# Optimization experiments

Hardware: AMD Instinct MI355X
Metric: run time of the kernel (lower is better)

## Reference

```python
import jax, jax.numpy as jnp
import numpy as np

C = 256
C4 = C // 4  # 64
B = 4
N = 4096
FACTOR = float(np.sqrt(C4))


def setup_inputs() -> dict:
    key = jax.random.key(0)
    k1, k2, k3, k4 = jax.random.split(key, 4)
    x = jax.random.normal(k1, (B, C, N), dtype=jnp.float32)
    # q_conv and k_conv share the SAME weight (tied in the torch module)
    W_qk = jax.random.normal(k2, (C4, C), dtype=jnp.float32) * (1.0 / np.sqrt(C))
    W_v = jax.random.normal(k3, (C4, C), dtype=jnp.float32) * (1.0 / np.sqrt(C))
    b_v = jax.random.normal(k4, (C4,), dtype=jnp.float32) * 0.01
    return {"x": x, "W_qk": W_qk, "W_v": W_v, "b_v": b_v}


def reference(x, W_qk, W_v, b_v):
    # Conv1d with kernel size 1 == per-position linear: [B,C,N] -> [B,C4,N]
    x_q = jnp.einsum('oc,bcn->bon', W_qk, x)          # [B, C4, N]
    x_k = x_q                                          # tied weights: k == q
    x_v = jnp.einsum('oc,bcn->bon', W_v, x) + b_v[None, :, None]  # [B, C4, N]
    # energy = x_k.permute(0,2,1) @ x_q : [B, N, N]
    energy = jnp.einsum('bcn,bcm->bnm', x_k, x_q) / FACTOR
    attention = jax.nn.softmax(energy, axis=-1)        # softmax over last dim
    x_r = jnp.einsum('bcn,bnm->bcm', x_v, attention)   # [B, C4, N]
    return x_r
```

## Files before the change

### kernel.cpp

```cpp
#include <hip/hip_runtime.h>


#define CC 256
#define C4C 64
#define NBATCH 4
#define NN 4096
#define QSCALE 0.42466089f
#define SHIFT2 12.0f

typedef _Float16 f16;
typedef _Float16 half2v __attribute__((ext_vector_type(2)));
typedef _Float16 half4 __attribute__((ext_vector_type(4)));
typedef _Float16 half8 __attribute__((ext_vector_type(8)));
typedef __fp16 fp16x2 __attribute__((ext_vector_type(2)));
typedef float floatx4 __attribute__((ext_vector_type(4)));

static __device__ __forceinline__ half2v pkrtz(float a, float b) {
  fp16x2 r = __builtin_amdgcn_cvt_pkrtz(a, b);
  return __builtin_bit_cast(half2v, r);
}

#define LOADQ(T, A0, A1)                                                   \
  { const f16* p_ = Qb + (size_t)(T) * 1024 + l * 8;                       \
    A0 = *(const half8*)(p_); A1 = *(const half8*)(p_ + 512); }

#define XT_PITCH 264
__global__ __launch_bounds__(256) void qv_kernel(
    const float* __restrict__ x, const float* __restrict__ Wqk,
    const float* __restrict__ Wv, const float* __restrict__ bv,
    f16* __restrict__ Qtb, float* __restrict__ V)
{
  __shared__ __align__(16) f16 xt[32][XT_PITCH];
  const int b = blockIdx.y;
  const int n0 = blockIdx.x * 32;
  const int tid = threadIdx.x;

  {
    const int nq = tid & 7;
    const int cb = tid >> 3;
    const int c = cb * 8;
    const float* xp = x + (size_t)b * CC * NN + n0 + nq * 4;
    float4 r[8];
#pragma unroll
    for (int j = 0; j < 8; ++j)
      r[j] = *(const float4*)(xp + (size_t)(c + j) * NN);
#pragma unroll
    for (int s = 0; s < 4; ++s) {
      half8 h;
#pragma unroll
      for (int j = 0; j < 8; ++j) h[j] = (f16)(((const float*)&r[j])[s]);
      *(half8*)(&xt[nq * 4 + s][c]) = h;
    }
  }

  const int w = tid >> 6, l = tid & 63, lr = l & 15, lg = l >> 4;
  const float* Wsrc = (w < 2) ? Wqk : Wv;
  const int ocb = (w & 1) * 32;
  half8 af[2][8];
#pragma unroll
  for (int t = 0; t < 2; ++t) {
    const float* wp = Wsrc + (size_t)(ocb + t * 16 + lr) * CC + 8 * lg;
#pragma unroll
    for (int kk = 0; kk < 8; ++kk) {
      float4 wa = *(const float4*)(wp + kk * 32);
      float4 wb = *(const float4*)(wp + kk * 32 + 4);
      half8 h;
      h[0] = (f16)wa.x; h[1] = (f16)wa.y; h[2] = (f16)wa.z; h[3] = (f16)wa.w;
      h[4] = (f16)wb.x; h[5] = (f16)wb.y; h[6] = (f16)wb.z; h[7] = (f16)wb.w;
      af[t][kk] = h;
    }
  }

  __syncthreads();

  floatx4 acc[2][2] = {{{0.f,0.f,0.f,0.f},{0.f,0.f,0.f,0.f}},
                       {{0.f,0.f,0.f,0.f},{0.f,0.f,0.f,0.f}}};
#pragma unroll
  for (int nt = 0; nt < 2; ++nt) {
#pragma unroll
    for (int kk = 0; kk < 8; ++kk) {
      half8 bf = *(const half8*)(&xt[nt * 16 + lr][kk * 32 + 8 * lg]);
      acc[0][nt] = __builtin_amdgcn_mfma_f32_16x16x32_f16(af[0][kk], bf, acc[0][nt], 0, 0, 0);
      acc[1][nt] = __builtin_amdgcn_mfma_f32_16x16x32_f16(af[1][kk], bf, acc[1][nt], 0, 0, 0);
    }
  }

  if (w < 2) {
#pragma unroll
    for (int t = 0; t < 2; ++t)
#pragma unroll
      for (int nt = 0; nt < 2; ++nt) {
        int T = (n0 >> 4) + nt;
        int kg = 2 * t + (lg >> 1);
        union { f16 h[4]; unsigned long long u; } q4;
#pragma unroll
        for (int i = 0; i < 4; ++i) q4.h[i] = (f16)(acc[t][nt][i] * QSCALE);
        *(unsigned long long*)(Qtb + (size_t)(b * 256 + T) * 1024 + w * 512
                               + (kg * 16 + lr) * 8 + (lg & 1) * 4) = q4.u;
      }
  } else {
#pragma unroll
    for (int t = 0; t < 2; ++t)
#pragma unroll
      for (int nt = 0; nt < 2; ++nt) {
        int n = n0 + nt * 16 + lr;
        int oc = (w - 2) * 32 + t * 16 + 4 * lg;
#pragma unroll
        for (int i = 0; i < 4; ++i)
          V[((size_t)(b * C4C) + oc + i) * NN + n] = acc[t][nt][i] + bv[oc + i];
      }
  }
}

#define Z_PRELOAD(TBEG)                                                    \
  { _Pragma("unroll")                                                      \
    for (int mt = 0; mt < 8; ++mt) {                                       \
      const f16* p_ = Qb + (size_t)((TBEG) + mt) * 1024 + l * 8;           \
      bb[mt][0] = *(const half8*)(p_);                                     \
      bb[mt][1] = *(const half8*)(p_ + 512);                               \
    } }

#define Z_E(MT, D0, D1)                                                    \
  { D0 = (floatx4){0.f,0.f,0.f,0.f}; D1 = (floatx4){0.f,0.f,0.f,0.f};      \
    D0 = __builtin_amdgcn_mfma_f32_16x16x32_f16(a[0][0], bb[MT][0], D0, 0, 0, 0); \
    D1 = __builtin_amdgcn_mfma_f32_16x16x32_f16(a[1][0], bb[MT][0], D1, 0, 0, 0); \
    D0 = __builtin_amdgcn_mfma_f32_16x16x32_f16(a[0][1], bb[MT][1], D0, 0, 0, 0); \
    D1 = __builtin_amdgcn_mfma_f32_16x16x32_f16(a[1][1], bb[MT][1], D1, 0, 0, 0); }

#define Z_SM(D0, D1)                                                       \
  { _Pragma("unroll")                                                      \
    for (int i = 0; i < 4; ++i) {                                          \
      rs[0][i] += __builtin_amdgcn_exp2f(D0[i]);                           \
      rs[1][i] += __builtin_amdgcn_exp2f(D1[i]); } }

#define Z_TILES17                                                          \
  Z_E(1, dB0, dB1); Z_SM(dA0, dA1);                                        \
  Z_E(2, dA0, dA1); Z_SM(dB0, dB1);                                        \
  Z_E(3, dB0, dB1); Z_SM(dA0, dA1);                                        \
  Z_E(4, dA0, dA1); Z_SM(dB0, dB1);                                        \
  Z_E(5, dB0, dB1); Z_SM(dA0, dA1);                                        \
  Z_E(6, dA0, dA1); Z_SM(dB0, dB1);                                        \
  Z_E(7, dB0, dB1); Z_SM(dA0, dA1);

__global__ __launch_bounds__(256) void z_kernel(
    const f16* __restrict__ Qtb, float* __restrict__ Zp)
{
  __shared__ float zl[4][32];
  const int bx = blockIdx.x;
  const int xcd = bx & 7, slot = bx >> 3;
  const int b = xcd >> 1;
  const int wu = ((xcd & 1) << 7) | slot;
  const int n0 = (wu >> 1) * 32;
  const int mh = wu & 1;
  const int tid = threadIdx.x;
  const int w = tid >> 6, l = tid & 63, lr = l & 15, lg = l >> 4;
  const f16* Qb = Qtb + (size_t)b * 256 * 1024;

  half8 a[2][2];
  LOADQ((n0 >> 4), a[0][0], a[0][1]);
  LOADQ((n0 >> 4) + 1, a[1][0], a[1][1]);

  const int tstr = mh * 128 + w * 32;
  half8 bb[8][2];
  floatx4 dA0, dA1, dB0, dB1;
  float rs[2][4] = {{0.f,0.f,0.f,0.f},{0.f,0.f,0.f,0.f}};

  Z_PRELOAD(tstr);
  Z_E(0, dA0, dA1);
  Z_TILES17;
#pragma unroll 1
  for (int mch = 1; mch < 4; ++mch) {
    Z_PRELOAD(tstr + mch * 8);
    Z_SM(dB0, dB1);
    Z_E(0, dA0, dA1);
    Z_TILES17;
  }
  Z_SM(dB0, dB1);

#pragma unroll
  for (int t = 0; t < 2; ++t)
#pragma unroll
    for (int i = 0; i < 4; ++i) {
      float v = rs[t][i];
      v += __shfl_xor(v, 1); v += __shfl_xor(v, 2);
      v += __shfl_xor(v, 4); v += __shfl_xor(v, 8);
      rs[t][i] = v;
    }
  if (lr == 0) {
#pragma unroll
    for (int t = 0; t < 2; ++t)
#pragma unroll
      for (int i = 0; i < 4; ++i)
        zl[w][16 * t + 4 * lg + i] = rs[t][i];
  }
  __syncthreads();
  if (tid < 32) {
    float s = zl[0][tid] + zl[1][tid] + zl[2][tid] + zl[3][tid];
    Zp[(size_t)mh * NBATCH * NN + b * NN + n0 + tid] = s;
  }
}

__global__ __launch_bounds__(256) void zr_kernel(
    const float* __restrict__ Zp, float* __restrict__ Z)
{
  int i = blockIdx.x * 256 + threadIdx.x;
  Z[i] = Zp[i] + Zp[(size_t)NBATCH * NN + i];
}

__global__ __launch_bounds__(256) void u_kernel(
    const float* __restrict__ V, const float* __restrict__ Z,
    f16* __restrict__ U4)
{
  size_t t = (size_t)blockIdx.x * 256 + threadIdx.x;
  size_t e = t * 8;
  int b = (int)(e >> 18);
  int c = (int)((e >> 12) & 63);
  int n = (int)(e & (NN - 1));
  const float* vp = V + (size_t)b * C4C * NN + (size_t)c * NN + n;
  float4 v0 = *(const float4*)(vp);
  float4 v1 = *(const float4*)(vp + 4);
  const float* zp = Z + b * NN + n;
  float4 z0 = *(const float4*)(zp);
  float4 z1 = *(const float4*)(zp + 4);
  half2v h0 = pkrtz(v0.x * 4096.0f / z0.x, v0.y * 4096.0f / z0.y);
  half2v h1 = pkrtz(v0.z * 4096.0f / z0.z, v0.w * 4096.0f / z0.w);
  half2v h2 = pkrtz(v1.x * 4096.0f / z1.x, v1.y * 4096.0f / z1.y);
  half2v h3 = pkrtz(v1.z * 4096.0f / z1.z, v1.w * 4096.0f / z1.w);
  half8 h = {h0[0], h0[1], h1[0], h1[1], h2[0], h2[1], h3[0], h3[1]};
  *(half8*)(U4 + (size_t)b * (C4C * NN) + (size_t)(n >> 4) * 1024 + c * 16 + (n & 15)) = h;
}

#define LOADU(NB, UA)                                                      \
  { const f16* up_ = Ub + (size_t)(NB) * 1024 + 4 * lg;                    \
    _Pragma("unroll")                                                      \
    for (int cs = 0; cs < 4; ++cs)                                         \
      UA[cs] = *(const half4*)(up_ + (16 * cs + lr) * 16); }

__global__ __launch_bounds__(512, 4) void av_kernel(
    const f16* __restrict__ Qtb, const f16* __restrict__ U4,
    float* __restrict__ Out)
{
  __shared__ float red[8][2][16][17];

  const int bx = blockIdx.x;
  const int xcd = bx & 7, slot = bx >> 3;
  const int b = xcd >> 1;
  const int m0 = (((xcd & 1) << 6) | slot) * 32;
  const int tid = threadIdx.x;
  const int w = tid >> 6;
  const int l = tid & 63;
  const int lr = l & 15, lg = l >> 4;

  const f16* Qb = Qtb + (size_t)b * 256 * 1024;
  const f16* Ub = U4 + (size_t)b * (C4C * NN);

  half8 bq[2][2];
  LOADQ((m0 >> 4), bq[0][0], bq[0][1]);
  LOADQ((m0 >> 4) + 1, bq[1][0], bq[1][1]);

  floatx4 o[4][2];
#pragma unroll
  for (int cs = 0; cs < 4; ++cs)
#pragma unroll
    for (int t = 0; t < 2; ++t) o[cs][t] = (floatx4){0.f, 0.f, 0.f, 0.f};

#pragma unroll 2
  for (int it = 0; it < 32; ++it) {
    const int T = it * 8 + w;
    half8 a0, a1;
    LOADQ(T, a0, a1);
    half4 ua[4];
    LOADU(T, ua);

    floatx4 dA = {-SHIFT2, -SHIFT2, -SHIFT2, -SHIFT2};
    floatx4 dB = {-SHIFT2, -SHIFT2, -SHIFT2, -SHIFT2};
    dA = __builtin_amdgcn_mfma_f32_16x16x32_f16(a0, bq[0][0], dA, 0, 0, 0);
    dB = __builtin_amdgcn_mfma_f32_16x16x32_f16(a0, bq[1][0], dB, 0, 0, 0);
    dA = __builtin_amdgcn_mfma_f32_16x16x32_f16(a1, bq[0][1], dA, 0, 0, 0);
    dB = __builtin_amdgcn_mfma_f32_16x16x32_f16(a1, bq[1][1], dB, 0, 0, 0);

    half2v p0a = pkrtz(__builtin_amdgcn_exp2f(dA[0]), __builtin_amdgcn_exp2f(dA[1]));
    half2v p0b = pkrtz(__builtin_amdgcn_exp2f(dA[2]), __builtin_amdgcn_exp2f(dA[3]));
    half2v p1a = pkrtz(__builtin_amdgcn_exp2f(dB[0]), __builtin_amdgcn_exp2f(dB[1]));
    half2v p1b = pkrtz(__builtin_amdgcn_exp2f(dB[2]), __builtin_amdgcn_exp2f(dB[3]));
    half4 bt0 = {p0a[0], p0a[1], p0b[0], p0b[1]};
    half4 bt1 = {p1a[0], p1a[1], p1b[0], p1b[1]};
#pragma unroll
    for (int cs = 0; cs < 4; ++cs) {
      o[cs][0] = __builtin_amdgcn_mfma_f32_16x16x16f16(ua[cs], bt0, o[cs][0], 0, 0, 0);
      o[cs][1] = __builtin_amdgcn_mfma_f32_16x16x16f16(ua[cs], bt1, o[cs][1], 0, 0, 0);
    }
  }

#pragma unroll 1
  for (int cs = 0; cs < 4; ++cs) {
    __syncthreads();
#pragma unroll
    for (int t = 0; t < 2; ++t)
#pragma unroll
      for (int i = 0; i < 4; ++i)
        red[w][t][4 * lg + i][lr] = o[cs][t][i];
    __syncthreads();
    const int t = tid >> 8;
    const int r = (tid >> 4) & 15;
    const int col = tid & 15;
    float ssum = 0.f;
#pragma unroll
    for (int ww = 0; ww < 8; ++ww) ssum += red[ww][t][r][col];
    Out[((size_t)b * C4C + cs * 16 + r) * NN + m0 + t * 16 + col] = ssum;
  }
}

extern "C" void kernel_launch(void* const* d_in, const int* in_sizes, int n_in,
                              void* d_out, int out_size, void* d_ws, size_t ws_size,
                              hipStream_t stream)
{
  const float* x   = (const float*)d_in[0];
  const float* Wqk = (const float*)d_in[1];
  const float* Wv  = (const float*)d_in[2];
  const float* bv  = (const float*)d_in[3];
  float* out = (float*)d_out;

  char* ws = (char*)d_ws;
  f16*   Qtb = (f16*)(ws);
  float* V   = (float*)(ws + (2u << 20));
  float* Z   = (float*)(ws + (6u << 20));
  f16*   U4  = (f16*)(ws + (6u << 20) + (64u << 10));
  float* Zp  = (float*)(ws + (6u << 20) + (64u << 10));

  qv_kernel<<<dim3(128, 4), 256, 0, stream>>>(x, Wqk, Wv, bv, Qtb, V);
  z_kernel<<<dim3(1024), 256, 0, stream>>>(Qtb, Zp);
  zr_kernel<<<dim3(64), 256, 0, stream>>>(Zp, Z);
  u_kernel<<<dim3(512), 256, 0, stream>>>(V, Z, U4);
  av_kernel<<<dim3(512), 512, 0, stream>>>(Qtb, U4, out);
}
```

Before: 64.98 us.

## Retile z_kernel to 64 rows per block with four-way column split

Each z_kernel block now covers 64 query rows (four 16-row tiles held in registers) and a quarter of the key columns, instead of 32 rows and half the columns. Each loaded key tile is reused across four A tiles, which raises MFMA work per global load. The zr_kernel now sums four partial Z arrays instead of two. The explicit software pipelining of the MFMA and exp2 steps is dropped in favour of a simple loop, and more registers are held live, which could reduce overlap or occupancy.

After: 67.52 us. +3.9%, slower.

```diff
diff --git a/kernel.cpp b/kernel.cpp
--- a/kernel.cpp
+++ b/kernel.cpp
@@ -112,73 +112,55 @@
   }
 }
 
-#define Z_PRELOAD(TBEG)                                                    \
-  { _Pragma("unroll")                                                      \
-    for (int mt = 0; mt < 8; ++mt) {                                       \
-      const f16* p_ = Qb + (size_t)((TBEG) + mt) * 1024 + l * 8;           \
-      bb[mt][0] = *(const half8*)(p_);                                     \
-      bb[mt][1] = *(const half8*)(p_ + 512);                               \
-    } }
-
-#define Z_E(MT, D0, D1)                                                    \
-  { D0 = (floatx4){0.f,0.f,0.f,0.f}; D1 = (floatx4){0.f,0.f,0.f,0.f};      \
-    D0 = __builtin_amdgcn_mfma_f32_16x16x32_f16(a[0][0], bb[MT][0], D0, 0, 0, 0); \
-    D1 = __builtin_amdgcn_mfma_f32_16x16x32_f16(a[1][0], bb[MT][0], D1, 0, 0, 0); \
-    D0 = __builtin_amdgcn_mfma_f32_16x16x32_f16(a[0][1], bb[MT][1], D0, 0, 0, 0); \
-    D1 = __builtin_amdgcn_mfma_f32_16x16x32_f16(a[1][1], bb[MT][1], D1, 0, 0, 0); }
-
-#define Z_SM(D0, D1)                                                       \
-  { _Pragma("unroll")                                                      \
-    for (int i = 0; i < 4; ++i) {                                          \
-      rs[0][i] += __builtin_amdgcn_exp2f(D0[i]);                           \
-      rs[1][i] += __builtin_amdgcn_exp2f(D1[i]); } }
-
-#define Z_TILES17                                                          \
-  Z_E(1, dB0, dB1); Z_SM(dA0, dA1);                                        \
-  Z_E(2, dA0, dA1); Z_SM(dB0, dB1);                                        \
-  Z_E(3, dB0, dB1); Z_SM(dA0, dA1);                                        \
-  Z_E(4, dA0, dA1); Z_SM(dB0, dB1);                                        \
-  Z_E(5, dB0, dB1); Z_SM(dA0, dA1);                                        \
-  Z_E(6, dA0, dA1); Z_SM(dB0, dB1);                                        \
-  Z_E(7, dB0, dB1); Z_SM(dA0, dA1);
-
 __global__ __launch_bounds__(256) void z_kernel(
     const f16* __restrict__ Qtb, float* __restrict__ Zp)
 {
-  __shared__ float zl[4][32];
+  __shared__ float zl[4][64];
   const int bx = blockIdx.x;
   const int xcd = bx & 7, slot = bx >> 3;
   const int b = xcd >> 1;
   const int wu = ((xcd & 1) << 7) | slot;
-  const int n0 = (wu >> 1) * 32;
-  const int mh = wu & 1;
+  const int n0t = (wu >> 2) * 4;
+  const int mq = wu & 3;
   const int tid = threadIdx.x;
   const int w = tid >> 6, l = tid & 63, lr = l & 15, lg = l >> 4;
   const f16* Qb = Qtb + (size_t)b * 256 * 1024;
 
-  half8 a[2][2];
-  LOADQ((n0 >> 4), a[0][0], a[0][1]);
-  LOADQ((n0 >> 4) + 1, a[1][0], a[1][1]);
-
-  const int tstr = mh * 128 + w * 32;
-  half8 bb[8][2];
-  floatx4 dA0, dA1, dB0, dB1;
-  float rs[2][4] = {{0.f,0.f,0.f,0.f},{0.f,0.f,0.f,0.f}};
-
-  Z_PRELOAD(tstr);
-  Z_E(0, dA0, dA1);
-  Z_TILES17;
+  half8 a[4][2];
+#pragma unroll
+  for (int t = 0; t < 4; ++t) LOADQ(n0t + t, a[t][0], a[t][1]);
+
+  const int tstr = mq * 64 + w * 16;
+  float rs[4][4];
+#pragma unroll
+  for (int t = 0; t < 4; ++t)
+#pragma unroll
+    for (int i = 0; i < 4; ++i) rs[t][i] = 0.f;
+
 #pragma unroll 1
-  for (int mch = 1; mch < 4; ++mch) {
-    Z_PRELOAD(tstr + mch * 8);
-    Z_SM(dB0, dB1);
-    Z_E(0, dA0, dA1);
-    Z_TILES17;
-  }
-  Z_SM(dB0, dB1);
-
-#pragma unroll
-  for (int t = 0; t < 2; ++t)
+  for (int ch = 0; ch < 2; ++ch) {
+    half8 bb[8][2];
+#pragma unroll
+    for (int mt = 0; mt < 8; ++mt) {
+      const f16* p_ = Qb + (size_t)(tstr + ch * 8 + mt) * 1024 + l * 8;
+      bb[mt][0] = *(const half8*)(p_);
+      bb[mt][1] = *(const half8*)(p_ + 512);
+    }
+#pragma unroll
+    for (int mt = 0; mt < 8; ++mt) {
+#pragma unroll
+      for (int t = 0; t < 4; ++t) {
+        floatx4 d = {0.f, 0.f, 0.f, 0.f};
+        d = __builtin_amdgcn_mfma_f32_16x16x32_f16(a[t][0], bb[mt][0], d, 0, 0, 0);
+        d = __builtin_amdgcn_mfma_f32_16x16x32_f16(a[t][1], bb[mt][1], d, 0, 0, 0);
+#pragma unroll
+        for (int i = 0; i < 4; ++i) rs[t][i] += __builtin_amdgcn_exp2f(d[i]);
+      }
+    }
+  }
+
+#pragma unroll
+  for (int t = 0; t < 4; ++t)
 #pragma unroll
     for (int i = 0; i < 4; ++i) {
       float v = rs[t][i];
@@ -188,15 +170,15 @@
     }
   if (lr == 0) {
 #pragma unroll
-    for (int t = 0; t < 2; ++t)
+    for (int t = 0; t < 4; ++t)
 #pragma unroll
       for (int i = 0; i < 4; ++i)
         zl[w][16 * t + 4 * lg + i] = rs[t][i];
   }
   __syncthreads();
-  if (tid < 32) {
+  if (tid < 64) {
     float s = zl[0][tid] + zl[1][tid] + zl[2][tid] + zl[3][tid];
-    Zp[(size_t)mh * NBATCH * NN + b * NN + n0 + tid] = s;
+    Zp[(size_t)mq * NBATCH * NN + b * NN + n0t * 16 + tid] = s;
   }
 }
 
@@ -204,7 +186,10 @@
     const float* __restrict__ Zp, float* __restrict__ Z)
 {
   int i = blockIdx.x * 256 + threadIdx.x;
-  Z[i] = Zp[i] + Zp[(size_t)NBATCH * NN + i];
+  float s = 0.f;
+#pragma unroll
+  for (int k = 0; k < 4; ++k) s += Zp[(size_t)k * NBATCH * NN + i];
+  Z[i] = s;
 }
 
 __global__ __launch_bounds__(256) void u_kernel(
```

## Fold softmax normalization into P and drop the separate U kernel

Applied to the files above, without the earlier changes.

The qv kernel now writes V directly as fp16 in the tiled layout the attention kernel consumes. The zr kernel produces a scaled reciprocal of the softmax denominator, and the av kernel multiplies each exp2 value by it before converting to fp16. This removes the u_kernel launch and its fp32 V round trip, at the cost of an extra float4 load and four multiplies per iteration in the hot loop. It also changes where normalization rounding happens: V is now rounded to fp16 unnormalized, which may shift precision slightly.

Measured after the change: 63.03 us. -3.0%, faster.

```diff
diff --git a/kernel.cpp b/kernel.cpp
--- a/kernel.cpp
+++ b/kernel.cpp
@@ -28,7 +28,7 @@
 __global__ __launch_bounds__(256) void qv_kernel(
     const float* __restrict__ x, const float* __restrict__ Wqk,
     const float* __restrict__ Wv, const float* __restrict__ bv,
-    f16* __restrict__ Qtb, float* __restrict__ V)
+    f16* __restrict__ Qtb, f16* __restrict__ V4)
 {
   __shared__ __align__(16) f16 xt[32][XT_PITCH];
   const int b = blockIdx.y;
@@ -103,11 +103,12 @@
     for (int t = 0; t < 2; ++t)
 #pragma unroll
       for (int nt = 0; nt < 2; ++nt) {
-        int n = n0 + nt * 16 + lr;
+        int T = (n0 >> 4) + nt;
         int oc = (w - 2) * 32 + t * 16 + 4 * lg;
 #pragma unroll
         for (int i = 0; i < 4; ++i)
-          V[((size_t)(b * C4C) + oc + i) * NN + n] = acc[t][nt][i] + bv[oc + i];
+          V4[(size_t)(b * 256 + T) * 1024 + (oc + i) * 16 + lr] =
+              (f16)(acc[t][nt][i] + bv[oc + i]);
       }
   }
 }
@@ -201,44 +202,21 @@
 }
 
 __global__ __launch_bounds__(256) void zr_kernel(
-    const float* __restrict__ Zp, float* __restrict__ Z)
+    const float* __restrict__ Zp, float* __restrict__ Zinv)
 {
   int i = blockIdx.x * 256 + threadIdx.x;
-  Z[i] = Zp[i] + Zp[(size_t)NBATCH * NN + i];
-}
-
-__global__ __launch_bounds__(256) void u_kernel(
-    const float* __restrict__ V, const float* __restrict__ Z,
-    f16* __restrict__ U4)
-{
-  size_t t = (size_t)blockIdx.x * 256 + threadIdx.x;
-  size_t e = t * 8;
-  int b = (int)(e >> 18);
-  int c = (int)((e >> 12) & 63);
-  int n = (int)(e & (NN - 1));
-  const float* vp = V + (size_t)b * C4C * NN + (size_t)c * NN + n;
-  float4 v0 = *(const float4*)(vp);
-  float4 v1 = *(const float4*)(vp + 4);
-  const float* zp = Z + b * NN + n;
-  float4 z0 = *(const float4*)(zp);
-  float4 z1 = *(const float4*)(zp + 4);
-  half2v h0 = pkrtz(v0.x * 4096.0f / z0.x, v0.y * 4096.0f / z0.y);
-  half2v h1 = pkrtz(v0.z * 4096.0f / z0.z, v0.w * 4096.0f / z0.w);
-  half2v h2 = pkrtz(v1.x * 4096.0f / z1.x, v1.y * 4096.0f / z1.y);
-  half2v h3 = pkrtz(v1.z * 4096.0f / z1.z, v1.w * 4096.0f / z1.w);
-  half8 h = {h0[0], h0[1], h1[0], h1[1], h2[0], h2[1], h3[0], h3[1]};
-  *(half8*)(U4 + (size_t)b * (C4C * NN) + (size_t)(n >> 4) * 1024 + c * 16 + (n & 15)) = h;
-}
-
-#define LOADU(NB, UA)                                                      \
-  { const f16* up_ = Ub + (size_t)(NB) * 1024 + 4 * lg;                    \
+  Zinv[i] = 4096.0f / (Zp[i] + Zp[(size_t)NBATCH * NN + i]);
+}
+
+#define LOADV(NB, UA)                                                      \
+  { const f16* up_ = Vb + (size_t)(NB) * 1024 + 4 * lg;                    \
     _Pragma("unroll")                                                      \
     for (int cs = 0; cs < 4; ++cs)                                         \
       UA[cs] = *(const half4*)(up_ + (16 * cs + lr) * 16); }
 
 __global__ __launch_bounds__(512, 4) void av_kernel(
-    const f16* __restrict__ Qtb, const f16* __restrict__ U4,
-    float* __restrict__ Out)
+    const f16* __restrict__ Qtb, const f16* __restrict__ V4,
+    const float* __restrict__ Zinv, float* __restrict__ Out)
 {
   __shared__ float red[8][2][16][17];
 
@@ -252,7 +230,8 @@
   const int lr = l & 15, lg = l >> 4;
 
   const f16* Qb = Qtb + (size_t)b * 256 * 1024;
-  const f16* Ub = U4 + (size_t)b * (C4C * NN);
+  const f16* Vb = V4 + (size_t)b * 256 * 1024;
+  const float* Zb = Zinv + b * NN;
 
   half8 bq[2][2];
   LOADQ((m0 >> 4), bq[0][0], bq[0][1]);
@@ -269,8 +248,9 @@
     const int T = it * 8 + w;
     half8 a0, a1;
     LOADQ(T, a0, a1);
-    half4 ua[4];
-    LOADU(T, ua);
+    half4 va[4];
+    LOADV(T, va);
+    const float4 zi = *(const float4*)(Zb + T * 16 + 4 * lg);
 
     floatx4 dA = {-SHIFT2, -SHIFT2, -SHIFT2, -SHIFT2};
     floatx4 dB = {-SHIFT2, -SHIFT2, -SHIFT2, -SHIFT2};
@@ -279,16 +259,20 @@
     dA = __builtin_amdgcn_mfma_f32_16x16x32_f16(a1, bq[0][1], dA, 0, 0, 0);
     dB = __builtin_amdgcn_mfma_f32_16x16x32_f16(a1, bq[1][1], dB, 0, 0, 0);
 
-    half2v p0a = pkrtz(__builtin_amdgcn_exp2f(dA[0]), __builtin_amdgcn_exp2f(dA[1]));
-    half2v p0b = pkrtz(__builtin_amdgcn_exp2f(dA[2]), __builtin_amdgcn_exp2f(dA[3]));
-    half2v p1a = pkrtz(__builtin_amdgcn_exp2f(dB[0]), __builtin_amdgcn_exp2f(dB[1]));
-    half2v p1b = pkrtz(__builtin_amdgcn_exp2f(dB[2]), __builtin_amdgcn_exp2f(dB[3]));
+    half2v p0a = pkrtz(__builtin_amdgcn_exp2f(dA[0]) * zi.x,
+                       __builtin_amdgcn_exp2f(dA[1]) * zi.y);
+    half2v p0b = pkrtz(__builtin_amdgcn_exp2f(dA[2]) * zi.z,
+                       __builtin_amdgcn_exp2f(dA[3]) * zi.w);
+    half2v p1a = pkrtz(__builtin_amdgcn_exp2f(dB[0]) * zi.x,
+                       __builtin_amdgcn_exp2f(dB[1]) * zi.y);
+    half2v p1b = pkrtz(__builtin_amdgcn_exp2f(dB[2]) * zi.z,
+                       __builtin_amdgcn_exp2f(dB[3]) * zi.w);
     half4 bt0 = {p0a[0], p0a[1], p0b[0], p0b[1]};
     half4 bt1 = {p1a[0], p1a[1], p1b[0], p1b[1]};
 #pragma unroll
     for (int cs = 0; cs < 4; ++cs) {
-      o[cs][0] = __builtin_amdgcn_mfma_f32_16x16x16f16(ua[cs], bt0, o[cs][0], 0, 0, 0);
-      o[cs][1] = __builtin_amdgcn_mfma_f32_16x16x16f16(ua[cs], bt1, o[cs][1], 0, 0, 0);
+      o[cs][0] = __builtin_amdgcn_mfma_f32_16x16x16f16(va[cs], bt0, o[cs][0], 0, 0, 0);
+      o[cs][1] = __builtin_amdgcn_mfma_f32_16x16x16f16(va[cs], bt1, o[cs][1], 0, 0, 0);
     }
   }
 
@@ -322,15 +306,13 @@
   float* out = (float*)d_out;
 
   char* ws = (char*)d_ws;
-  f16*   Qtb = (f16*)(ws);
-  float* V   = (float*)(ws + (2u << 20));
-  float* Z   = (float*)(ws + (6u << 20));
-  f16*   U4  = (f16*)(ws + (6u << 20) + (64u << 10));
-  float* Zp  = (float*)(ws + (6u << 20) + (64u << 10));
-
-  qv_kernel<<<dim3(128, 4), 256, 0, stream>>>(x, Wqk, Wv, bv, Qtb, V);
+  f16*   Qtb  = (f16*)(ws);
+  f16*   V4   = (f16*)(ws + (2u << 20));
+  float* Zp   = (float*)(ws + (4u << 20));
+  float* Zinv = (float*)(ws + (4u << 20) + (128u << 10));
+
+  qv_kernel<<<dim3(128, 4), 256, 0, stream>>>(x, Wqk, Wv, bv, Qtb, V4);
   z_kernel<<<dim3(1024), 256, 0, stream>>>(Qtb, Zp);
-  zr_kernel<<<dim3(64), 256, 0, stream>>>(Zp, Z);
-  u_kernel<<<dim3(512), 256, 0, stream>>>(V, Z, U4);
-  av_kernel<<<dim3(512), 512, 0, stream>>>(Qtb, U4, out);
-}
+  zr_kernel<<<dim3(64), 256, 0, stream>>>(Zp, Zinv);
+  av_kernel<<<dim3(512), 512, 0, stream>>>(Qtb, V4, Zinv, out);
+}
```
